# Kernel optimization log

Hardware: AMD Instinct MI355X
Metric: run time of the kernel (lower is better)

## Reference

```python
import jax, jax.numpy as jnp
import numpy as np

N_NODE = 40000
EMB = 100
LAYERS = 2
B = 512
L = 50
N = 50
E = 800000


def _l2norm(x, axis=-1, eps=1e-12):
    n = jnp.sqrt(jnp.sum(x * x, axis=axis, keepdims=True))
    return x / jnp.maximum(n, eps)


def _item_conv(rows, cols, vals, emb, b):
    # sparse A @ X repeated LAYERS times, stack, l2-normalize rows, weighted sum
    finals = [emb]
    x = emb
    for _ in range(LAYERS):
        x = jax.ops.segment_sum(vals[:, None] * x[cols], rows, num_segments=emb.shape[0])
        finals.append(x)
    f = _l2norm(jnp.stack(finals, 0))                      # [LAYERS+1, n, d]
    return jnp.sum(b[:, None, None] * f, axis=0)


def _session_conv(adj_dense, emb, a):
    finals = [emb]
    x = emb
    for _ in range(LAYERS):
        x = adj_dense @ x
        finals.append(x)
    f = _l2norm(jnp.stack(finals, 0))
    return jnp.sum(a[:, None, None] * f, axis=0)


def _gat(h, adj, a0, a1, a2, a3):
    # e_k[b,i,j] = leakyrelu(sum_d h[b,i,d]*h[b,j,d]*a_k[d]); never materialize [B,N,N,D]
    def score(a):
        return jax.nn.leaky_relu(jnp.einsum('bid,bjd->bij', h * a[:, 0], h), 0.2)
    e0, e1, e2, e3 = score(a0), score(a1), score(a2), score(a3)
    neg = jnp.float32(-9e15)
    alpha = jnp.where(adj == 1, e0, neg)
    alpha = jnp.where(adj == 2, e1, alpha)
    alpha = jnp.where(adj == 3, e2, alpha)
    alpha = jnp.where(adj == 4, e3, alpha)
    alpha = jax.nn.softmax(alpha, axis=-1)
    return jnp.einsum('bij,bjd->bid', alpha, h)


def _get_seq(emb_table, rev, h, alias, mix=0.8):
    seq_h = emb_table[rev]                                  # [B,L,D]
    bidx = jnp.arange(rev.shape[0])[:, None]
    seq_h_ = h[bidx, alias]                                 # [B,L,D]
    return (1.0 - mix) * seq_h + mix * seq_h_               # eval: dropout = identity


def _soft_attention(seq_h, mask_f, session_len, pos_emb, w1_W, w1_b, glu1_W, glu1_b, glu2_W, w2):
    hs = jnp.sum(seq_h, axis=1) / session_len               # [B,D]
    pos = jnp.broadcast_to(pos_emb[:seq_h.shape[1]][None], seq_h.shape)
    nh = jnp.tanh(jnp.concatenate([pos, seq_h], -1) @ w1_W.T + w1_b)
    nh = jax.nn.sigmoid(nh @ glu1_W.T + glu1_b + (hs @ glu2_W.T)[:, None, :])
    beta = (nh @ w2) * mask_f[..., None]                    # [B,L,1]
    return jnp.sum(beta * seq_h, axis=1)                    # [B,D]


def setup_inputs() -> dict:
    key = jax.random.key(0)
    ks = jax.random.split(key, 30)
    stdv = 1.0 / np.sqrt(EMB)
    u = lambda k, s: jax.random.uniform(k, s, jnp.float32, -stdv, stdv)
    return {
        'tar': jax.random.randint(ks[0], (B,), 0, N_NODE),
        'reversed_sess_item': jax.random.randint(ks[1], (B, L), 0, N_NODE + 1),
        'mask': jnp.ones((B, L), jnp.int32),
        'session_len': jnp.ones((B, 1), jnp.float32),
        'session_adj': jax.random.uniform(ks[2], (B, B), jnp.float32),
        'is_train': 0,
        'items': jax.random.randint(ks[3], (B, N), 0, N_NODE + 1),
        'adj': jax.random.randint(ks[4], (B, N, N), 0, 5),
        'alias_session': jax.random.randint(ks[5], (B, L), 0, N),
        'gnn_rows': jax.random.randint(ks[6], (E,), 0, N_NODE),
        'gnn_cols': jax.random.randint(ks[7], (E,), 0, N_NODE),
        'gnn_vals': jax.random.uniform(ks[8], (E,), jnp.float32),
        'nodes_emb': u(ks[9], (N_NODE, EMB)),
        'b_item': jnp.ones((LAYERS + 1,), jnp.float32),
        'a_sess': jnp.ones((LAYERS + 1,), jnp.float32),
        'a0': u(ks[10], (EMB, 1)), 'a1': u(ks[11], (EMB, 1)),
        'a2': u(ks[12], (EMB, 1)), 'a3': u(ks[13], (EMB, 1)),
        'w1_W': u(ks[14], (EMB, 2 * EMB)), 'w1_b': u(ks[15], (EMB,)),
        'w2': u(ks[16], (EMB, 1)),
        'glu1_W': u(ks[17], (EMB, EMB)), 'glu1_b': u(ks[18], (EMB,)),
        'glu2_W': u(ks[19], (EMB, EMB)),
        'pos_emb': u(ks[20], (150, EMB)),
    }


def reference(tar, reversed_sess_item, mask, session_len, session_adj, is_train,
              items, adj, alias_session, gnn_rows, gnn_cols, gnn_vals,
              nodes_emb, b_item, a_sess, a0, a1, a2, a3,
              w1_W, w1_b, w2, glu1_W, glu1_b, glu2_W, pos_emb):
    mask_f = mask.astype(jnp.float32)
    zeros = jnp.zeros((1, EMB), jnp.float32)
    emb_gnn = _item_conv(gnn_rows, gnn_cols, gnn_vals, nodes_emb, b_item)
    # eval mode: both dropouts are identity
    e1t = jnp.concatenate([zeros, emb_gnn], 0)
    e2t = jnp.concatenate([zeros, emb_gnn], 0)
    embeddings = e1t + e2t

    h1 = _gat(e1t[items], adj, a0, a1, a2, a3)
    h1 = _get_seq(e1t, reversed_sess_item, h1, alias_session, 0.8)
    h2 = _gat(e2t[items], adj, a0, a1, a2, a3)
    h2 = _get_seq(e2t, reversed_sess_item, h2, alias_session, 0.8)

    sel1 = _soft_attention(h1, mask_f, session_len, pos_emb, w1_W, w1_b, glu1_W, glu1_b, glu2_W, w2)
    sel1 = _session_conv(session_adj, sel1, a_sess)
    sel2 = _soft_attention(h2, mask_f, session_len, pos_emb, w1_W, w1_b, glu1_W, glu1_b, glu2_W, w2)
    sel2 = _session_conv(session_adj, sel2, a_sess)

    con_loss = jnp.float32(0.0)  # is_train == 0 (inference path)

    seq_h = sel1 + sel2
    scores = seq_h @ embeddings[1:].T                       # [B, N_NODE]
    logp = jax.nn.log_softmax(scores + 1e-8, axis=-1)
    loss = -jnp.mean(logp[jnp.arange(scores.shape[0]), tar])
    return (con_loss, loss, scores)
```

## Files before the change

### kernel.cpp

```cpp
#include <hip/hip_runtime.h>
#include <hip/hip_bf16.h>
#include <math.h>

#define N_NODE 40000
#define EMB 100
#define BB 512
#define LL 50
#define NI 50
#define EDG 800000
#define SCAN_BLOCKS 157

typedef short s16x8 __attribute__((ext_vector_type(8)));
typedef float f32x4 __attribute__((ext_vector_type(4)));

__global__ void khist(const int* __restrict__ rows, int* __restrict__ counts) {
  int e = blockIdx.x * 256 + threadIdx.x;
  atomicAdd(&counts[rows[e]], 1);
}

__global__ __launch_bounds__(256) void kscan1(const int* __restrict__ counts,
                                              int* __restrict__ scanout,
                                              int* __restrict__ blocksums, int n) {
  __shared__ int wsum[4];
  int tid = threadIdx.x;
  int i = blockIdx.x * 256 + tid;
  int v = (i < n) ? counts[i] : 0;
  int x = v;
  #pragma unroll
  for (int off = 1; off < 64; off <<= 1) {
    int t = __shfl_up(x, off, 64);
    if ((tid & 63) >= off) x += t;
  }
  int w = tid >> 6, lane = tid & 63;
  if (lane == 63) wsum[w] = x;
  __syncthreads();
  int woff = 0;
  #pragma unroll
  for (int k = 0; k < 4; ++k) woff += (k < w) ? wsum[k] : 0;
  int incl = x + woff;
  if (i < n) scanout[i] = incl - v;
  if (tid == 255) blocksums[blockIdx.x] = incl;
}

__global__ __launch_bounds__(256) void kscan2(int* __restrict__ blocksums, int nb) {
  __shared__ int wsum[4];
  int tid = threadIdx.x;
  int v = (tid < nb) ? blocksums[tid] : 0;
  int x = v;
  #pragma unroll
  for (int off = 1; off < 64; off <<= 1) {
    int t = __shfl_up(x, off, 64);
    if ((tid & 63) >= off) x += t;
  }
  int w = tid >> 6, lane = tid & 63;
  if (lane == 63) wsum[w] = x;
  __syncthreads();
  int woff = 0;
  #pragma unroll
  for (int k = 0; k < 4; ++k) woff += (k < w) ? wsum[k] : 0;
  if (tid < nb) blocksums[tid] = x + woff - v;
}

__global__ __launch_bounds__(256) void kscan3(const int* __restrict__ scanout,
                                              const int* __restrict__ blocksums,
                                              int* __restrict__ starts,
                                              int* __restrict__ cursor, int n) {
  int i = blockIdx.x * 256 + threadIdx.x;
  if (i < n) {
    int s = scanout[i] + blocksums[blockIdx.x];
    starts[i] = s;
    cursor[i] = s;
  }
}

__global__ void kfill(const int* __restrict__ rows, const int* __restrict__ cols,
                      const float* __restrict__ vals, int* __restrict__ cursor,
                      int* __restrict__ colS, float* __restrict__ valS) {
  int e = blockIdx.x * 256 + threadIdx.x;
  int r = rows[e];
  int p = atomicAdd(&cursor[r], 1);
  colS[p] = cols[e];
  valS[p] = vals[e];
}

__global__ __launch_bounds__(256) void kspmm(const int* __restrict__ starts,
                                             const int* __restrict__ counts,
                                             const int* __restrict__ colS,
                                             const float* __restrict__ valS,
                                             const float* __restrict__ x,
                                             float* __restrict__ out) {
  int row = blockIdx.x * 4 + (threadIdx.x >> 6);
  int lane = threadIdx.x & 63;
  int s = starts[row], cnt = counts[row];
  bool act = lane < 50;
  int d2 = (act ? lane : 49) * 2;
  float ax = 0.f, ay = 0.f;
  for (int base = 0; base < cnt; base += 64) {
    int nb = cnt - base; if (nb > 64) nb = 64;
    int cl = 0; float vl = 0.f;
    if (lane < nb) {
      cl = colS[s + base + lane];
      vl = valS[s + base + lane];
    }
    int t = 0;
    for (; t + 8 <= nb; t += 8) {
      int c0 = __shfl(cl, t),     c1 = __shfl(cl, t + 1);
      int c2 = __shfl(cl, t + 2), c3 = __shfl(cl, t + 3);
      int c4 = __shfl(cl, t + 4), c5 = __shfl(cl, t + 5);
      int c6 = __shfl(cl, t + 6), c7 = __shfl(cl, t + 7);
      float v0 = __shfl(vl, t),     v1 = __shfl(vl, t + 1);
      float v2 = __shfl(vl, t + 2), v3 = __shfl(vl, t + 3);
      float v4 = __shfl(vl, t + 4), v5 = __shfl(vl, t + 5);
      float v6 = __shfl(vl, t + 6), v7 = __shfl(vl, t + 7);
      float2 g0 = *(const float2*)(x + (size_t)c0 * EMB + d2);
      float2 g1 = *(const float2*)(x + (size_t)c1 * EMB + d2);
      float2 g2 = *(const float2*)(x + (size_t)c2 * EMB + d2);
      float2 g3 = *(const float2*)(x + (size_t)c3 * EMB + d2);
      float2 g4 = *(const float2*)(x + (size_t)c4 * EMB + d2);
      float2 g5 = *(const float2*)(x + (size_t)c5 * EMB + d2);
      float2 g6 = *(const float2*)(x + (size_t)c6 * EMB + d2);
      float2 g7 = *(const float2*)(x + (size_t)c7 * EMB + d2);
      ax += v0 * g0.x; ay += v0 * g0.y;
      ax += v1 * g1.x; ay += v1 * g1.y;
      ax += v2 * g2.x; ay += v2 * g2.y;
      ax += v3 * g3.x; ay += v3 * g3.y;
      ax += v4 * g4.x; ay += v4 * g4.y;
      ax += v5 * g5.x; ay += v5 * g5.y;
      ax += v6 * g6.x; ay += v6 * g6.y;
      ax += v7 * g7.x; ay += v7 * g7.y;
    }
    for (; t + 4 <= nb; t += 4) {
      int c0 = __shfl(cl, t),     c1 = __shfl(cl, t + 1);
      int c2 = __shfl(cl, t + 2), c3 = __shfl(cl, t + 3);
      float v0 = __shfl(vl, t),     v1 = __shfl(vl, t + 1);
      float v2 = __shfl(vl, t + 2), v3 = __shfl(vl, t + 3);
      float2 g0 = *(const float2*)(x + (size_t)c0 * EMB + d2);
      float2 g1 = *(const float2*)(x + (size_t)c1 * EMB + d2);
      float2 g2 = *(const float2*)(x + (size_t)c2 * EMB + d2);
      float2 g3 = *(const float2*)(x + (size_t)c3 * EMB + d2);
      ax += v0 * g0.x; ay += v0 * g0.y;
      ax += v1 * g1.x; ay += v1 * g1.y;
      ax += v2 * g2.x; ay += v2 * g2.y;
      ax += v3 * g3.x; ay += v3 * g3.y;
    }
    for (; t < nb; ++t) {
      int c = __shfl(cl, t);
      float v = __shfl(vl, t);
      float2 g = *(const float2*)(x + (size_t)c * EMB + d2);
      ax += v * g.x; ay += v * g.y;
    }
  }
  if (act) {
    float2 o; o.x = ax; o.y = ay;
    *(float2*)(out + (size_t)row * EMB + d2) = o;
  }
}

__global__ void kcomb(const float* __restrict__ x0, const float* __restrict__ x1,
                      const float* __restrict__ x2, const float* __restrict__ bI,
                      float* __restrict__ emb) {
  int n = blockIdx.x * 4 + (threadIdx.x >> 6);
  int lane = threadIdx.x & 63;
  int d0 = lane, d1 = lane + 64;
  bool h1 = d1 < EMB;
  size_t base = (size_t)n * EMB;
  float v00 = x0[base + d0], v01 = h1 ? x0[base + d1] : 0.f;
  float v10 = x1[base + d0], v11 = h1 ? x1[base + d1] : 0.f;
  float v20 = x2[base + d0], v21 = h1 ? x2[base + d1] : 0.f;
  float q0 = v00 * v00 + v01 * v01;
  float q1 = v10 * v10 + v11 * v11;
  float q2 = v20 * v20 + v21 * v21;
  #pragma unroll
  for (int off = 32; off; off >>= 1) {
    q0 += __shfl_xor(q0, off);
    q1 += __shfl_xor(q1, off);
    q2 += __shfl_xor(q2, off);
  }
  float r0 = 1.f / fmaxf(sqrtf(q0), 1e-12f);
  float r1 = 1.f / fmaxf(sqrtf(q1), 1e-12f);
  float r2 = 1.f / fmaxf(sqrtf(q2), 1e-12f);
  float b0 = bI[0], b1 = bI[1], b2 = bI[2];
  emb[base + d0] = b0 * v00 * r0 + b1 * v10 * r1 + b2 * v20 * r2;
  if (h1) emb[base + d1] = b0 * v01 * r0 + b1 * v11 * r1 + b2 * v21 * r2;
}

__global__ __launch_bounds__(256) void kgat(
    const float* __restrict__ emb, const int* __restrict__ items,
    const int* __restrict__ adj,
    const float* __restrict__ a0p, const float* __restrict__ a1p,
    const float* __restrict__ a2p, const float* __restrict__ a3p,
    float* __restrict__ hgat) {
  __shared__ __align__(16) float hl[64 * 108];
  __shared__ __align__(16) float as[4 * 100];
  __shared__ float alpha_lds[64 * 51];
  __shared__ float wred[4][2][64];
  int b = blockIdx.x;
  int tid = threadIdx.x;
  for (int idx = tid; idx < 400; idx += 256) {
    int k = idx / 100, d = idx % 100;
    const float* ap = (k == 0) ? a0p : (k == 1) ? a1p : (k == 2) ? a2p : a3p;
    as[idx] = ap[d];
  }
  for (int idx = tid; idx < 64 * 50; idx += 256) {
    int i = idx / 50, d2 = (idx % 50) * 2;
    float2 v; v.x = 0.f; v.y = 0.f;
    if (i < NI) {
      int node = items[b * NI + i];
      if (node != 0) v = *(const float2*)(emb + (size_t)(node - 1) * EMB + d2);
    }
    *(float2*)&hl[i * 108 + d2] = v;
  }
  __syncthreads();
  int w = tid >> 6, lane = tid & 63;
  int j0 = w * 13;
  int nj = 50 - j0; if (nj > 13) nj = 13;

  float4 hreg[25];
  #pragma unroll
  for (int q = 0; q < 25; ++q) hreg[q] = *(const float4*)&hl[lane * 108 + q * 4];

  int al_lane = (lane < NI) ? lane : NI - 1;
  const int* adjrow = adj + (size_t)b * (NI * NI) + al_lane * NI + j0;
  int adjv[13];
  #pragma unroll
  for (int t = 0; t < 13; ++t) adjv[t] = (t < nj) ? adjrow[t] : 0;

  float e[13];
  #pragma unroll
  for (int jj = 0; jj < 13; ++jj) {
    float acc = 0.f;
    if (jj < nj) {
      int j = j0 + jj;
      int k = adjv[jj] - 1; k = (k < 0) ? 0 : (k > 3) ? 3 : k;
      const float* aw = &as[k * 100];
      #pragma unroll
      for (int q = 0; q < 25; ++q) {
        float4 hj = *(const float4*)&hl[j * 108 + q * 4];
        float4 a4 = *(const float4*)(aw + q * 4);
        float4 hm = hreg[q];
        acc += hm.x * hj.x * a4.x + hm.y * hj.y * a4.y
             + hm.z * hj.z * a4.z + hm.w * hj.w * a4.w;
      }
      acc = (acc >= 0.f) ? acc : 0.2f * acc;
      acc = (adjv[jj] == 0) ? -9e15f : acc;
    } else {
      acc = -INFINITY;
    }
    e[jj] = acc;
  }

  float mloc = -INFINITY;
  #pragma unroll
  for (int jj = 0; jj < 13; ++jj) if (jj < nj) mloc = fmaxf(mloc, e[jj]);
  wred[w][0][lane] = mloc;
  __syncthreads();
  float m = fmaxf(fmaxf(wred[0][0][lane], wred[1][0][lane]),
                  fmaxf(wred[2][0][lane], wred[3][0][lane]));
  float sloc = 0.f;
  #pragma unroll
  for (int jj = 0; jj < 13; ++jj) if (jj < nj) {
    e[jj] = expf(e[jj] - m);
    sloc += e[jj];
  }
  wred[w][1][lane] = sloc;
  __syncthreads();
  float s = (wred[0][1][lane] + wred[1][1][lane]) +
            (wred[2][1][lane] + wred[3][1][lane]);
  float inv = 1.f / s;
  #pragma unroll
  for (int jj = 0; jj < 13; ++jj) if (jj < nj)
    alpha_lds[lane * 51 + j0 + jj] = e[jj] * inv;
  __syncthreads();

  int nq = (w == 0) ? 7 : 6;
  float4 outq[7];
  #pragma unroll
  for (int t = 0; t < 7; ++t) outq[t] = make_float4(0.f, 0.f, 0.f, 0.f);
  for (int j = 0; j < NI; ++j) {
    float aj = alpha_lds[lane * 51 + j];
    #pragma unroll
    for (int t = 0; t < 7; ++t) {
      if (t < nq) {
        int q = w + 4 * t;
        float4 hv = *(const float4*)&hl[j * 108 + q * 4];
        outq[t].x += aj * hv.x; outq[t].y += aj * hv.y;
        outq[t].z += aj * hv.z; outq[t].w += aj * hv.w;
      }
    }
  }
  if (lane < NI) {
    #pragma unroll
    for (int t = 0; t < 7; ++t) {
      if (t < nq) {
        int q = w + 4 * t;
        *(float4*)&hgat[((size_t)b * NI + lane) * EMB + q * 4] = outq[t];
      }
    }
  }
}

__global__ void kseq(const float* __restrict__ emb, const int* __restrict__ rev,
                     const int* __restrict__ alias, const float* __restrict__ hgat,
                     float* __restrict__ hseq) {
  int idx = blockIdx.x * 256 + threadIdx.x;
  int b = idx / 5000, r = idx % 5000, l = r / 100, d = r % 100;
  int node = rev[b * LL + l];
  float sh = (node == 0) ? 0.f : emb[(size_t)(node - 1) * EMB + d];
  int a = alias[b * LL + l];
  float shh = hgat[((size_t)b * NI + a) * EMB + d];
  hseq[idx] = 0.2f * sh + 0.8f * shh;
}

__global__ void kprep_t(const float* __restrict__ w1W, const float* __restrict__ g1W,
                        const float* __restrict__ g2W, float* __restrict__ w1t2,
                        float* __restrict__ g1t, float* __restrict__ g2t) {
  int idx = blockIdx.x * 256 + threadIdx.x;
  if (idx >= 10000) return;
  int c = idx / 100, o = idx % 100;
  w1t2[c * 100 + o] = w1W[o * 200 + 100 + c];
  g1t[c * 100 + o] = g1W[o * 100 + c];
  g2t[c * 100 + o] = g2W[o * 100 + c];
}

__global__ void kprep_pos(const float* __restrict__ posE, const float* __restrict__ w1W,
                          const float* __restrict__ w1b, float* __restrict__ posW) {
  int idx = blockIdx.x * 256 + threadIdx.x;
  if (idx >= 5000) return;
  int l = idx / 100, o = idx % 100;
  float acc = w1b[o];
  for (int c = 0; c < 100; ++c) acc += posE[l * 100 + c] * w1W[o * 200 + c];
  posW[idx] = acc;
}

__global__ __launch_bounds__(256) void ksoft(
    const float* __restrict__ hseqG, const float* __restrict__ slenp,
    const int* __restrict__ maskp,
    const float* __restrict__ posW, const float* __restrict__ w1t2,
    const float* __restrict__ glu1t, const float* __restrict__ glu1b,
    const float* __restrict__ glu2t, const float* __restrict__ w2,
    float* __restrict__ sel) {
  __shared__ float hq[LL * 101];
  __shared__ float nh[LL * 100];
  __shared__ float red[25 * 52];
  __shared__ float hs_s[100];
  __shared__ float g_s[100];
  __shared__ float beta_s[LL];
  int b = blockIdx.x, tid = threadIdx.x;
  for (int idx = tid; idx < LL * 100; idx += 256) {
    int l = idx / 100, d = idx % 100;
    hq[l * 101 + d] = hseqG[((size_t)b * LL + l) * 100 + d];
  }
  __syncthreads();
  if (tid < 100) {
    float s = 0.f;
    for (int l = 0; l < LL; ++l) s += hq[l * 101 + tid];
    hs_s[tid] = s / slenp[b];
  }
  __syncthreads();
  if (tid < 100) {
    float acc = 0.f;
    for (int c = 0; c < 100; ++c) acc += hs_s[c] * glu2t[c * 100 + tid];
    g_s[tid] = acc;
  }
  int lg = tid / 25, og = tid % 25;
  if (tid < 250) {
    float acc[5][4];
    #pragma unroll
    for (int j = 0; j < 5; ++j) {
      float4 p = *(const float4*)&posW[(lg * 5 + j) * 100 + og * 4];
      acc[j][0] = p.x; acc[j][1] = p.y; acc[j][2] = p.z; acc[j][3] = p.w;
    }
    for (int c = 0; c < 100; ++c) {
      float4 wv = *(const float4*)&w1t2[c * 100 + og * 4];
      float hv[5];
      #pragma unroll
      for (int j = 0; j < 5; ++j) hv[j] = hq[(lg * 5 + j) * 101 + c];
      #pragma unroll
      for (int j = 0; j < 5; ++j) {
        acc[j][0] += hv[j] * wv.x;
        acc[j][1] += hv[j] * wv.y;
        acc[j][2] += hv[j] * wv.z;
        acc[j][3] += hv[j] * wv.w;
      }
    }
    #pragma unroll
    for (int j = 0; j < 5; ++j) {
      float4 t;
      t.x = tanhf(acc[j][0]); t.y = tanhf(acc[j][1]);
      t.z = tanhf(acc[j][2]); t.w = tanhf(acc[j][3]);
      *(float4*)&nh[(lg * 5 + j) * 100 + og * 4] = t;
    }
  }
  __syncthreads();
  if (tid < 250) {
    float4 gb = *(const float4*)&glu1b[og * 4];
    float4 gg = *(const float4*)&g_s[og * 4];
    float base0 = gg.x + gb.x, base1 = gg.y + gb.y, base2 = gg.z + gb.z, base3 = gg.w + gb.w;
    float acc[5][4];
    #pragma unroll
    for (int j = 0; j < 5; ++j) {
      acc[j][0] = base0; acc[j][1] = base1; acc[j][2] = base2; acc[j][3] = base3;
    }
    for (int c = 0; c < 100; ++c) {
      float4 wv = *(const float4*)&glu1t[c * 100 + og * 4];
      float hv[5];
      #pragma unroll
      for (int j = 0; j < 5; ++j) hv[j] = nh[(lg * 5 + j) * 100 + c];
      #pragma unroll
      for (int j = 0; j < 5; ++j) {
        acc[j][0] += hv[j] * wv.x;
        acc[j][1] += hv[j] * wv.y;
        acc[j][2] += hv[j] * wv.z;
        acc[j][3] += hv[j] * wv.w;
      }
    }
    float4 w2v = *(const float4*)&w2[og * 4];
    #pragma unroll
    for (int j = 0; j < 5; ++j) {
      float s0 = w2v.x / (1.f + expf(-acc[j][0]));
      float s1 = w2v.y / (1.f + expf(-acc[j][1]));
      float s2 = w2v.z / (1.f + expf(-acc[j][2]));
      float s3 = w2v.w / (1.f + expf(-acc[j][3]));
      red[og * 52 + lg * 5 + j] = (s0 + s1) + (s2 + s3);
    }
  }
  __syncthreads();
  if (tid < LL) {
    float s = 0.f;
    for (int og2 = 0; og2 < 25; ++og2) s += red[og2 * 52 + tid];
    beta_s[tid] = s * (float)maskp[b * LL + tid];
  }
  __syncthreads();
  if (tid < 100) {
    float acc = 0.f;
    for (int l = 0; l < LL; ++l) acc += beta_s[l] * hq[l * 101 + tid];
    sel[(size_t)b * 100 + tid] = acc;
  }
}

__global__ void ksess(const float* __restrict__ adjS, const float* __restrict__ x,
                      float* __restrict__ out) {
  int b = blockIdx.x, d = threadIdx.x;
  if (d >= 100) return;
  const float* ar = adjS + (size_t)b * BB;
  float a0 = 0.f, a1 = 0.f, a2 = 0.f, a3 = 0.f;
  for (int j = 0; j < BB; j += 4) {
    a0 += ar[j]     * x[(j)     * 100 + d];
    a1 += ar[j + 1] * x[(j + 1) * 100 + d];
    a2 += ar[j + 2] * x[(j + 2) * 100 + d];
    a3 += ar[j + 3] * x[(j + 3) * 100 + d];
  }
  out[(size_t)b * 100 + d] = (a0 + a1) + (a2 + a3);
}

__global__ void ksesscomb(const float* __restrict__ x0, const float* __restrict__ x1,
                          const float* __restrict__ x2, const float* __restrict__ aS,
                          float* __restrict__ out) {
  int b = blockIdx.x * 4 + (threadIdx.x >> 6);
  int lane = threadIdx.x & 63;
  int d0 = lane, d1 = lane + 64;
  bool h1 = d1 < EMB;
  size_t base = (size_t)b * EMB;
  float v00 = x0[base + d0], v01 = h1 ? x0[base + d1] : 0.f;
  float v10 = x1[base + d0], v11 = h1 ? x1[base + d1] : 0.f;
  float v20 = x2[base + d0], v21 = h1 ? x2[base + d1] : 0.f;
  float q0 = v00 * v00 + v01 * v01;
  float q1 = v10 * v10 + v11 * v11;
  float q2 = v20 * v20 + v21 * v21;
  #pragma unroll
  for (int off = 32; off; off >>= 1) {
    q0 += __shfl_xor(q0, off);
    q1 += __shfl_xor(q1, off);
    q2 += __shfl_xor(q2, off);
  }
  float r0 = 1.f / fmaxf(sqrtf(q0), 1e-12f);
  float r1 = 1.f / fmaxf(sqrtf(q1), 1e-12f);
  float r2 = 1.f / fmaxf(sqrtf(q2), 1e-12f);
  float b0 = aS[0], b1 = aS[1], b2 = aS[2];
  out[base + d0] = 2.f * (b0 * v00 * r0 + b1 * v10 * r1 + b2 * v20 * r2);
  if (h1) out[base + d1] = 2.f * (b0 * v01 * r0 + b1 * v11 * r1 + b2 * v21 * r2);
}

__global__ void kprepB(const float* __restrict__ emb, unsigned short* __restrict__ bHi,
                       unsigned short* __restrict__ bLo) {
  int idx = blockIdx.x * 256 + threadIdx.x;
  int n = idx >> 7, k = idx & 127;
  float v = (k < EMB) ? 2.f * emb[(size_t)n * EMB + k] : 0.f;
  __hip_bfloat16 h = __float2bfloat16(v);
  float rem = v - __bfloat162float(h);
  __hip_bfloat16 l = __float2bfloat16(rem);
  bHi[idx] = *reinterpret_cast<unsigned short*>(&h);
  bLo[idx] = *reinterpret_cast<unsigned short*>(&l);
}

__global__ void kprepA(const float* __restrict__ seqh, unsigned short* __restrict__ aHi,
                       unsigned short* __restrict__ aLo) {
  int idx = blockIdx.x * 256 + threadIdx.x;
  int n = idx >> 7, k = idx & 127;
  float v = (k < EMB) ? seqh[(size_t)n * EMB + k] : 0.f;
  __hip_bfloat16 h = __float2bfloat16(v);
  float rem = v - __bfloat162float(h);
  __hip_bfloat16 l = __float2bfloat16(rem);
  aHi[idx] = *reinterpret_cast<unsigned short*>(&h);
  aLo[idx] = *reinterpret_cast<unsigned short*>(&l);
}

__global__ __launch_bounds__(256) void kscoresM(
    const unsigned short* __restrict__ aHi, const unsigned short* __restrict__ aLo,
    const unsigned short* __restrict__ bHi, const unsigned short* __restrict__ bLo,
    float* __restrict__ outS) {
  __shared__ __align__(16) unsigned short Bh[64 * 136];
  __shared__ __align__(16) unsigned short Bl[64 * 136];
  int tid = threadIdx.x;
  int n0 = blockIdx.x * 64, b0 = blockIdx.y * 64;
  int w = tid >> 6, lane = tid & 63;
  int ln = lane & 15, quad = lane >> 4;

  const unsigned short* aRowH = aHi + (size_t)(b0 + w * 16 + ln) * 128 + quad * 8;
  const unsigned short* aRowL = aLo + (size_t)(b0 + w * 16 + ln) * 128 + quad * 8;
  s16x8 ah[4], al[4];
  #pragma unroll
  for (int s = 0; s < 4; ++s) {
    ah[s] = *(const s16x8*)(aRowH + s * 32);
    al[s] = *(const s16x8*)(aRowL + s * 32);
  }

  #pragma unroll
  for (int it = 0; it < 4; ++it) {
    int seg = tid + it * 256;
    int r = seg >> 4, q = seg & 15;
    *(s16x8*)&Bh[r * 136 + q * 8] = *(const s16x8*)&bHi[(size_t)(n0 + r) * 128 + q * 8];
    *(s16x8*)&Bl[r * 136 + q * 8] = *(const s16x8*)&bLo[(size_t)(n0 + r) * 128 + q * 8];
  }
  __syncthreads();

  f32x4 acc[4];
  #pragma unroll
  for (int t = 0; t < 4; ++t) acc[t] = (f32x4){0.f, 0.f, 0.f, 0.f};

  #pragma unroll
  for (int s = 0; s < 4; ++s) {
    #pragma unroll
    for (int t = 0; t < 4; ++t) {
      s16x8 bh = *(const s16x8*)&Bh[(t * 16 + ln) * 136 + s * 32 + quad * 8];
      s16x8 bl = *(const s16x8*)&Bl[(t * 16 + ln) * 136 + s * 32 + quad * 8];
      acc[t] = __builtin_amdgcn_mfma_f32_16x16x32_bf16(ah[s], bh, acc[t], 0, 0, 0);
      acc[t] = __builtin_amdgcn_mfma_f32_16x16x32_bf16(al[s], bh, acc[t], 0, 0, 0);
      acc[t] = __builtin_amdgcn_mfma_f32_16x16x32_bf16(ah[s], bl, acc[t], 0, 0, 0);
    }
  }

  int brow = b0 + w * 16 + quad * 4;
  #pragma unroll
  for (int t = 0; t < 4; ++t) {
    int ncol = n0 + t * 16 + ln;
    #pragma unroll
    for (int r = 0; r < 4; ++r) {
      outS[(size_t)(brow + r) * N_NODE + ncol] = acc[t][r];
    }
  }
}

__global__ __launch_bounds__(256) void klse(const float* __restrict__ outS,
                                            const int* __restrict__ tar,
                                            float* __restrict__ part) {
  __shared__ float ms[256], ss[256];
  int b = blockIdx.x, tid = threadIdx.x;
  const float2* sp = (const float2*)(outS + (size_t)b * N_NODE);
  float m = -INFINITY, s = 0.f;
  for (int i = tid; i < N_NODE / 2; i += 256) {
    float2 v = sp[i];
    float mx = fmaxf(v.x, v.y);
    float add = expf(v.x - mx) + expf(v.y - mx);
    if (mx > m) { s = s * expf(m - mx) + add; m = mx; }
    else s += add * expf(mx - m);
  }
  ms[tid] = m; ss[tid] = s;
  __syncthreads();
  for (int st = 128; st; st >>= 1) {
    if (tid < st) {
      float m2 = ms[tid + st], s2 = ss[tid + st];
      float M = fmaxf(ms[tid], m2);
      ss[tid] = ss[tid] * expf(ms[tid] - M) + s2 * expf(m2 - M);
      ms[tid] = M;
    }
    __syncthreads();
  }
  if (tid == 0) {
    float tsc = outS[(size_t)b * N_NODE + tar[b]];
    part[b] = tsc - (ms[0] + logf(ss[0]));
  }
}

__global__ void kfinal(const float* __restrict__ part, float* __restrict__ out) {
  __shared__ float red[256];
  int tid = threadIdx.x;
  red[tid] = part[tid] + part[tid + 256];
  __syncthreads();
  for (int st = 128; st; st >>= 1) {
    if (tid < st) red[tid] += red[tid + st];
    __syncthreads();
  }
  if (tid == 0) {
    out[0] = 0.f;
    out[1] = -red[0] / (float)BB;
  }
}

extern "C" void kernel_launch(void* const* d_in, const int* in_sizes, int n_in,
                              void* d_out, int out_size, void* d_ws, size_t ws_size,
                              hipStream_t stream) {
  const int* tar    = (const int*)d_in[0];
  const int* rev    = (const int*)d_in[1];
  const int* maskp  = (const int*)d_in[2];
  const float* slen = (const float*)d_in[3];
  const float* sadj = (const float*)d_in[4];
  const int* items  = (const int*)d_in[6];
  const int* adjp   = (const int*)d_in[7];
  const int* alias  = (const int*)d_in[8];
  const int* grows  = (const int*)d_in[9];
  const int* gcols  = (const int*)d_in[10];
  const float* gvals = (const float*)d_in[11];
  const float* nemb = (const float*)d_in[12];
  const float* bI   = (const float*)d_in[13];
  const float* aS   = (const float*)d_in[14];
  const float* a0p  = (const float*)d_in[15];
  const float* a1p  = (const float*)d_in[16];
  const float* a2p  = (const float*)d_in[17];
  const float* a3p  = (const float*)d_in[18];
  const float* w1W  = (const float*)d_in[19];
  const float* w1b  = (const float*)d_in[20];
  const float* w2p  = (const float*)d_in[21];
  const float* g1W  = (const float*)d_in[22];
  const float* g1b  = (const float*)d_in[23];
  const float* g2W  = (const float*)d_in[24];
  const float* posE = (const float*)d_in[25];

  float* W = (float*)d_ws;
  size_t o = 0;
  float* emb_gnn = W + o; o += (size_t)N_NODE * EMB;
  float* x1      = W + o; o += (size_t)N_NODE * EMB;
  float* x2      = W + o; o += (size_t)N_NODE * EMB;
  float* sel     = W + o; o += (size_t)BB * EMB;
  float* y1      = W + o; o += (size_t)BB * EMB;
  float* y2      = W + o; o += (size_t)BB * EMB;
  float* seqh    = W + o; o += (size_t)BB * EMB;
  float* posW    = W + o; o += 5120;
  float* w1t2    = W + o; o += 10000;
  float* glu1t   = W + o; o += 10000;
  float* glu2t   = W + o; o += 10000;
  float* valS    = W + o; o += EDG;
  float* part    = W + o; o += 512;
  int* colS   = (int*)(W + o); o += EDG;
  int* counts = (int*)(W + o); o += N_NODE;
  int* starts = (int*)(W + o); o += N_NODE;
  int* cursor = (int*)(W + o); o += N_NODE;
  int* scantmp = (int*)(W + o); o += N_NODE;
  int* blocksums = (int*)(W + o); o += 256;
  unsigned short* aHi = (unsigned short*)(W + o); o += 32768;
  unsigned short* aLo = (unsigned short*)(W + o); o += 32768;
  float* hgat = x1;
  float* hseq = x2;
  unsigned short* bHi = (unsigned short*)x1;
  unsigned short* bLo = (unsigned short*)x2;

  float* outF = (float*)d_out;
  float* outScores = outF + 2;

  hipMemsetAsync(counts, 0, N_NODE * sizeof(int), stream);
  khist<<<EDG / 256, 256, 0, stream>>>(grows, counts);
  kscan1<<<SCAN_BLOCKS, 256, 0, stream>>>(counts, scantmp, blocksums, N_NODE);
  kscan2<<<1, 256, 0, stream>>>(blocksums, SCAN_BLOCKS);
  kscan3<<<SCAN_BLOCKS, 256, 0, stream>>>(scantmp, blocksums, starts, cursor, N_NODE);
  kfill<<<EDG / 256, 256, 0, stream>>>(grows, gcols, gvals, cursor, colS, valS);
  kspmm<<<N_NODE / 4, 256, 0, stream>>>(starts, counts, colS, valS, nemb, x1);
  kspmm<<<N_NODE / 4, 256, 0, stream>>>(starts, counts, colS, valS, x1, x2);
  kcomb<<<N_NODE / 4, 256, 0, stream>>>(nemb, x1, x2, bI, emb_gnn);
  kgat<<<BB, 256, 0, stream>>>(emb_gnn, items, adjp, a0p, a1p, a2p, a3p, hgat);
  kseq<<<(BB * LL * EMB) / 256, 256, 0, stream>>>(emb_gnn, rev, alias, hgat, hseq);
  kprep_t<<<40, 256, 0, stream>>>(w1W, g1W, g2W, w1t2, glu1t, glu2t);
  kprep_pos<<<20, 256, 0, stream>>>(posE, w1W, w1b, posW);
  ksoft<<<BB, 256, 0, stream>>>(hseq, slen, maskp, posW, w1t2, glu1t, g1b, glu2t, w2p, sel);
  kprepB<<<(N_NODE * 128) / 256, 256, 0, stream>>>(emb_gnn, bHi, bLo);
  ksess<<<BB, 128, 0, stream>>>(sadj, sel, y1);
  ksess<<<BB, 128, 0, stream>>>(sadj, y1, y2);
  ksesscomb<<<BB / 4, 256, 0, stream>>>(sel, y1, y2, aS, seqh);
  kprepA<<<(BB * 128) / 256, 256, 0, stream>>>(seqh, aHi, aLo);
  kscoresM<<<dim3(N_NODE / 64, BB / 64), 256, 0, stream>>>(aHi, aLo, bHi, bLo, outScores);
  klse<<<BB, 256, 0, stream>>>(outScores, tar, part);
  kfinal<<<1, 256, 0, stream>>>(part, outF);
}
```

Before: 544.3 us.

## Interleave CSR col/val storage and loop batch tiles inside scores kernel

The CSR fill now writes column index and value as one interleaved int2 array, with each thread handling four edges, so kspmm reads both with a single 8-byte load. The scores GEMM switches from a 2D grid of 64x64 tiles to a 1D grid of 32-node tiles. Each block loads its B tile into shared memory once and loops over all 512 batch rows, which cuts repeated B tile loads. The cost is fewer blocks (1250) each doing more serial work, and narrower 32-column stores.

```diff
diff --git a/kernel.cpp b/kernel.cpp
--- a/kernel.cpp
+++ b/kernel.cpp
@@ -73,20 +73,27 @@
   }
 }
 
-__global__ void kfill(const int* __restrict__ rows, const int* __restrict__ cols,
-                      const float* __restrict__ vals, int* __restrict__ cursor,
-                      int* __restrict__ colS, float* __restrict__ valS) {
-  int e = blockIdx.x * 256 + threadIdx.x;
-  int r = rows[e];
-  int p = atomicAdd(&cursor[r], 1);
-  colS[p] = cols[e];
-  valS[p] = vals[e];
+__global__ __launch_bounds__(256) void kfill(const int* __restrict__ rows,
+                                             const int* __restrict__ cols,
+                                             const float* __restrict__ vals,
+                                             int* __restrict__ cursor,
+                                             int2* __restrict__ colval) {
+  int e0 = (blockIdx.x * 256 + threadIdx.x) * 4;
+  #pragma unroll
+  for (int k = 0; k < 4; ++k) {
+    int e = e0 + k;
+    if (e < EDG) {
+      int r = rows[e];
+      int p = atomicAdd(&cursor[r], 1);
+      int2 cv; cv.x = cols[e]; cv.y = __float_as_int(vals[e]);
+      colval[p] = cv;
+    }
+  }
 }
 
 __global__ __launch_bounds__(256) void kspmm(const int* __restrict__ starts,
                                              const int* __restrict__ counts,
-                                             const int* __restrict__ colS,
-                                             const float* __restrict__ valS,
+                                             const int2* __restrict__ colval,
                                              const float* __restrict__ x,
                                              float* __restrict__ out) {
   int row = blockIdx.x * 4 + (threadIdx.x >> 6);
@@ -99,8 +106,8 @@
     int nb = cnt - base; if (nb > 64) nb = 64;
     int cl = 0; float vl = 0.f;
     if (lane < nb) {
-      cl = colS[s + base + lane];
-      vl = valS[s + base + lane];
+      int2 cv = colval[s + base + lane];
+      cl = cv.x; vl = __int_as_float(cv.y);
     }
     int t = 0;
     for (; t + 8 <= nb; t += 8) {
@@ -509,24 +516,15 @@
     const unsigned short* __restrict__ aHi, const unsigned short* __restrict__ aLo,
     const unsigned short* __restrict__ bHi, const unsigned short* __restrict__ bLo,
     float* __restrict__ outS) {
-  __shared__ __align__(16) unsigned short Bh[64 * 136];
-  __shared__ __align__(16) unsigned short Bl[64 * 136];
+  __shared__ __align__(16) unsigned short Bh[32 * 136];
+  __shared__ __align__(16) unsigned short Bl[32 * 136];
   int tid = threadIdx.x;
-  int n0 = blockIdx.x * 64, b0 = blockIdx.y * 64;
+  int n0 = blockIdx.x * 32;
   int w = tid >> 6, lane = tid & 63;
   int ln = lane & 15, quad = lane >> 4;
 
-  const unsigned short* aRowH = aHi + (size_t)(b0 + w * 16 + ln) * 128 + quad * 8;
-  const unsigned short* aRowL = aLo + (size_t)(b0 + w * 16 + ln) * 128 + quad * 8;
-  s16x8 ah[4], al[4];
-  #pragma unroll
-  for (int s = 0; s < 4; ++s) {
-    ah[s] = *(const s16x8*)(aRowH + s * 32);
-    al[s] = *(const s16x8*)(aRowL + s * 32);
-  }
-
-  #pragma unroll
-  for (int it = 0; it < 4; ++it) {
+  #pragma unroll
+  for (int it = 0; it < 2; ++it) {
     int seg = tid + it * 256;
     int r = seg >> 4, q = seg & 15;
     *(s16x8*)&Bh[r * 136 + q * 8] = *(const s16x8*)&bHi[(size_t)(n0 + r) * 128 + q * 8];
@@ -534,29 +532,37 @@
   }
   __syncthreads();
 
-  f32x4 acc[4];
-  #pragma unroll
-  for (int t = 0; t < 4; ++t) acc[t] = (f32x4){0.f, 0.f, 0.f, 0.f};
-
-  #pragma unroll
-  for (int s = 0; s < 4; ++s) {
-    #pragma unroll
-    for (int t = 0; t < 4; ++t) {
-      s16x8 bh = *(const s16x8*)&Bh[(t * 16 + ln) * 136 + s * 32 + quad * 8];
-      s16x8 bl = *(const s16x8*)&Bl[(t * 16 + ln) * 136 + s * 32 + quad * 8];
-      acc[t] = __builtin_amdgcn_mfma_f32_16x16x32_bf16(ah[s], bh, acc[t], 0, 0, 0);
-      acc[t] = __builtin_amdgcn_mfma_f32_16x16x32_bf16(al[s], bh, acc[t], 0, 0, 0);
-      acc[t] = __builtin_amdgcn_mfma_f32_16x16x32_bf16(ah[s], bl, acc[t], 0, 0, 0);
-    }
-  }
-
-  int brow = b0 + w * 16 + quad * 4;
-  #pragma unroll
-  for (int t = 0; t < 4; ++t) {
-    int ncol = n0 + t * 16 + ln;
-    #pragma unroll
-    for (int r = 0; r < 4; ++r) {
-      outS[(size_t)(brow + r) * N_NODE + ncol] = acc[t][r];
+  for (int b0 = 0; b0 < BB; b0 += 64) {
+    const unsigned short* aRowH = aHi + (size_t)(b0 + w * 16 + ln) * 128 + quad * 8;
+    const unsigned short* aRowL = aLo + (size_t)(b0 + w * 16 + ln) * 128 + quad * 8;
+    s16x8 ah[4], al[4];
+    #pragma unroll
+    for (int s = 0; s < 4; ++s) {
+      ah[s] = *(const s16x8*)(aRowH + s * 32);
+      al[s] = *(const s16x8*)(aRowL + s * 32);
+    }
+    f32x4 acc[2];
+    #pragma unroll
+    for (int t = 0; t < 2; ++t) acc[t] = (f32x4){0.f, 0.f, 0.f, 0.f};
+    #pragma unroll
+    for (int s = 0; s < 4; ++s) {
+      #pragma unroll
+      for (int t = 0; t < 2; ++t) {
+        s16x8 bh = *(const s16x8*)&Bh[(t * 16 + ln) * 136 + s * 32 + quad * 8];
+        s16x8 bl = *(const s16x8*)&Bl[(t * 16 + ln) * 136 + s * 32 + quad * 8];
+        acc[t] = __builtin_amdgcn_mfma_f32_16x16x32_bf16(ah[s], bh, acc[t], 0, 0, 0);
+        acc[t] = __builtin_amdgcn_mfma_f32_16x16x32_bf16(al[s], bh, acc[t], 0, 0, 0);
+        acc[t] = __builtin_amdgcn_mfma_f32_16x16x32_bf16(ah[s], bl, acc[t], 0, 0, 0);
+      }
+    }
+    int brow = b0 + w * 16 + quad * 4;
+    #pragma unroll
+    for (int t = 0; t < 2; ++t) {
+      int ncol = n0 + t * 16 + ln;
+      #pragma unroll
+      for (int r = 0; r < 4; ++r) {
+        outS[(size_t)(brow + r) * N_NODE + ncol] = acc[t][r];
+      }
     }
   }
 }
@@ -649,9 +655,8 @@
   float* w1t2    = W + o; o += 10000;
   float* glu1t   = W + o; o += 10000;
   float* glu2t   = W + o; o += 10000;
-  float* valS    = W + o; o += EDG;
+  int2* colval   = (int2*)(W + o); o += (size_t)2 * EDG;
   float* part    = W + o; o += 512;
-  int* colS   = (int*)(W + o); o += EDG;
   int* counts = (int*)(W + o); o += N_NODE;
   int* starts = (int*)(W + o); o += N_NODE;
   int* cursor = (int*)(W + o); o += N_NODE;
@@ -672,9 +677,9 @@
   kscan1<<<SCAN_BLOCKS, 256, 0, stream>>>(counts, scantmp, blocksums, N_NODE);
   kscan2<<<1, 256, 0, stream>>>(blocksums, SCAN_BLOCKS);
   kscan3<<<SCAN_BLOCKS, 256, 0, stream>>>(scantmp, blocksums, starts, cursor, N_NODE);
-  kfill<<<EDG / 256, 256, 0, stream>>>(grows, gcols, gvals, cursor, colS, valS);
-  kspmm<<<N_NODE / 4, 256, 0, stream>>>(starts, counts, colS, valS, nemb, x1);
-  kspmm<<<N_NODE / 4, 256, 0, stream>>>(starts, counts, colS, valS, x1, x2);
+  kfill<<<(EDG + 1023) / 1024, 256, 0, stream>>>(grows, gcols, gvals, cursor, colval);
+  kspmm<<<N_NODE / 4, 256, 0, stream>>>(starts, counts, colval, nemb, x1);
+  kspmm<<<N_NODE / 4, 256, 0, stream>>>(starts, counts, colval, x1, x2);
   kcomb<<<N_NODE / 4, 256, 0, stream>>>(nemb, x1, x2, bI, emb_gnn);
   kgat<<<BB, 256, 0, stream>>>(emb_gnn, items, adjp, a0p, a1p, a2p, a3p, hgat);
   kseq<<<(BB * LL * EMB) / 256, 256, 0, stream>>>(emb_gnn, rev, alias, hgat, hseq);
@@ -686,7 +691,7 @@
   ksess<<<BB, 128, 0, stream>>>(sadj, y1, y2);
   ksesscomb<<<BB / 4, 256, 0, stream>>>(sel, y1, y2, aS, seqh);
   kprepA<<<(BB * 128) / 256, 256, 0, stream>>>(seqh, aHi, aLo);
-  kscoresM<<<dim3(N_NODE / 64, BB / 64), 256, 0, stream>>>(aHi, aLo, bHi, bLo, outScores);
+  kscoresM<<<N_NODE / 32, 256, 0, stream>>>(aHi, aLo, bHi, bLo, outScores);
   klse<<<BB, 256, 0, stream>>>(outScores, tar, part);
   kfinal<<<1, 256, 0, stream>>>(part, outF);
 }
```

Result: slower. 560.5 us (+3.0%).
